# Kernel optimization log

Measured on AMD Instinct MI355X. Metric: run time of the kernel, lower is better.

## Reference

```python
import jax, jax.numpy as jnp
import numpy as np

N_NODES, N_EDGES, NODE_D, EDGE_D, EMB_D, N_GRAPHS = 50000, 800000, 128, 100, 92, 256
N_CONV, FC_D, N_FC, CUTOFF = 3, 128, 2, 6.0


def setup_inputs() -> dict:
    key = jax.random.key(0)
    ks = jax.random.split(key, 24)
    s = 0.05
    inp = {
        "z": jax.random.randint(ks[0], (N_NODES,), 0, 100, dtype=jnp.int32),
        "R": jax.random.normal(ks[1], (N_NODES, 3), dtype=jnp.float32) * 5.0,
        "edge_index": jax.random.randint(ks[2], (2, N_EDGES), 0, N_NODES, dtype=jnp.int32),
        "batch": jnp.sort(jax.random.randint(ks[3], (N_NODES,), 0, N_GRAPHS, dtype=jnp.int32)),
        # learned parameters
        "embedding": jax.random.uniform(ks[4], (100, EMB_D), dtype=jnp.float32),
        "emb_w": jax.random.normal(ks[5], (EMB_D, NODE_D), dtype=jnp.float32) * s,
        "emb_b": jnp.zeros((NODE_D,), jnp.float32),
        "conv_w": jax.random.normal(ks[6], (N_CONV, 2 * NODE_D + EDGE_D, 2 * NODE_D), dtype=jnp.float32) * s,
        "conv_b": jnp.zeros((N_CONV, 2 * NODE_D), jnp.float32),
        "ln_g": jnp.ones((N_CONV, NODE_D), jnp.float32),
        "ln_b": jnp.zeros((N_CONV, NODE_D), jnp.float32),
        "cfc_w": jax.random.normal(ks[7], (NODE_D, FC_D), dtype=jnp.float32) * s,
        "cfc_b": jnp.zeros((FC_D,), jnp.float32),
        "fc_w": jax.random.normal(ks[8], (N_FC, FC_D, FC_D), dtype=jnp.float32) * s,
        "fc_b": jnp.zeros((N_FC, FC_D), jnp.float32),
        "out_w": jax.random.normal(ks[9], (FC_D, 1), dtype=jnp.float32) * s,
        "out_b": jnp.zeros((1,), jnp.float32),
    }
    return inp


def _gaussian_smearing(d):
    offsets = jnp.linspace(0.0, CUTOFF, EDGE_D, dtype=d.dtype)  # [EDGE_D]
    coeff = -0.5 / (offsets[1] - offsets[0]) ** 2
    return jnp.exp(coeff * (d[:, None] - offsets[None, :]) ** 2)  # [E, EDGE_D]


def _layernorm(x, g, b, eps=1e-5):
    mu = x.mean(-1, keepdims=True)
    var = x.var(-1, keepdims=True)
    return (x - mu) / jnp.sqrt(var + eps) * g + b


def reference(z, R, edge_index, batch, embedding, emb_w, emb_b, conv_w, conv_b,
              ln_g, ln_b, cfc_w, cfc_b, fc_w, fc_b, out_w, out_b):
    src, dst = edge_index[0], edge_index[1]  # messages flow src(j) -> dst(i)
    d = jnp.linalg.norm(R[src] - R[dst], axis=-1)  # [E]
    edge_attr = _gaussian_smearing(d)  # [E, EDGE_D]

    x = embedding[z] @ emb_w + emb_b  # [N, NODE_D]
    n = x.shape[0]
    for l in range(conv_w.shape[0]):
        xi, xj = x[dst], x[src]  # gather [E, NODE_D]
        zc = jnp.concatenate([xi, xj, edge_attr], axis=1) @ conv_w[l] + conv_b[l]  # [E, 2*NODE_D]
        z1, z2 = jnp.split(zc, 2, axis=1)
        msg = jax.nn.sigmoid(z1) * jax.nn.softplus(z2)  # [E, NODE_D]
        agg = jax.ops.segment_sum(msg, dst, num_segments=n)  # scatter-add
        x = jax.nn.softplus(_layernorm(agg, ln_g[l], ln_b[l]) + x)

    # global mean pool over graphs
    sums = jax.ops.segment_sum(x, batch, num_segments=N_GRAPHS)
    cnts = jax.ops.segment_sum(jnp.ones((n, 1), x.dtype), batch, num_segments=N_GRAPHS)
    mol = sums / jnp.maximum(cnts, 1.0)  # [N_GRAPHS, NODE_D]

    h = jax.nn.softplus(mol @ cfc_w + cfc_b)
    for l in range(fc_w.shape[0]):
        h = jax.nn.softplus(h @ fc_w[l] + fc_b[l])
    return h @ out_w + out_b  # energy [N_GRAPHS, 1]
```

## Files before the change

kernel.cpp:

```cpp
#include <hip/hip_runtime.h>
#include <hip/hip_bf16.h>
#include <cmath>

#define N_NODES 50000
#define N_EDGES 800000
#define NODE_DIM 128
#define EDGE_DIM 100
#define EMB_DIM 92
#define N_GRAPHS 256

typedef __attribute__((ext_vector_type(8))) short short8_t;
typedef __attribute__((ext_vector_type(4))) float float4_t;

__device__ __forceinline__ float softplus_f(float v) {
    return v > 20.0f ? v : __logf(1.0f + __expf(v));
}
__device__ __forceinline__ float sigmoid_f(float v) {
    return 1.0f / (1.0f + __expf(-v));
}

__global__ void deg_kernel(const int* __restrict__ ei, int* __restrict__ deg) {
    int e = blockIdx.x * blockDim.x + threadIdx.x;
    if (e >= N_EDGES) return;
    atomicAdd(&deg[ei[N_EDGES + e]], 1);
}

#define SB 1024
__global__ void scan1_kernel(const int* __restrict__ deg, int* __restrict__ rp,
                             int* __restrict__ bsum) {
    __shared__ int buf[SB];
    int b = blockIdx.x, t = threadIdx.x, i = b * SB + t;
    int v = (i < N_NODES) ? deg[i] : 0;
    buf[t] = v;
    __syncthreads();
    for (int off = 1; off < SB; off <<= 1) {
        int a = (t >= off) ? buf[t - off] : 0;
        __syncthreads();
        buf[t] += a;
        __syncthreads();
    }
    if (i < N_NODES) rp[i] = buf[t] - v;
    if (t == SB - 1) bsum[b] = buf[t];
}
__global__ void scan2_kernel(int* __restrict__ bsum, int n) {
    if (threadIdx.x == 0) {
        int s = 0;
        for (int i = 0; i < n; i++) { int v = bsum[i]; bsum[i] = s; s += v; }
    }
}
__global__ void scan3_kernel(int* __restrict__ rp, const int* __restrict__ bsum) {
    int i = blockIdx.x * SB + threadIdx.x;
    if (i < N_NODES) rp[i] += bsum[blockIdx.x];
    if (i == 0) rp[N_NODES] = N_EDGES;
}

__global__ void fill_kernel(const int* __restrict__ ei, const float* __restrict__ R,
                            const int* __restrict__ row_ptr, int* __restrict__ cnt2,
                            int* __restrict__ s_src, float* __restrict__ s_d) {
    int e = blockIdx.x * blockDim.x + threadIdx.x;
    if (e >= N_EDGES) return;
    int s = ei[e];
    int dst = ei[N_EDGES + e];
    float dx = R[3 * s + 0] - R[3 * dst + 0];
    float dy = R[3 * s + 1] - R[3 * dst + 1];
    float dz = R[3 * s + 2] - R[3 * dst + 2];
    float d = sqrtf(dx * dx + dy * dy + dz * dz);
    int pos = row_ptr[dst] + atomicAdd(&cnt2[dst], 1);
    s_src[pos] = s;
    s_d[pos] = d;
}

__global__ void gb_kernel(const int* __restrict__ batch, int* __restrict__ gs) {
    int i = blockIdx.x * 256 + threadIdx.x;
    if (i > N_NODES) return;
    int b = (i < N_NODES) ? batch[i] : N_GRAPHS;
    int pb = (i == 0) ? -1 : batch[i - 1];
    for (int g = pb + 1; g <= b; g++) gs[g] = i;
}

__global__ void wcvt_kernel(const float* __restrict__ conv_w, __hip_bfloat16* __restrict__ Webf) {
    int i = blockIdx.x * 256 + threadIdx.x;
    if (i >= 3 * EDGE_DIM * 256) return;
    int l = i / (EDGE_DIM * 256), r = i - l * (EDGE_DIM * 256);
    Webf[i] = (__hip_bfloat16)conv_w[(size_t)l * 356 * 256 + 256 * 256 + r];
}

__global__ void wprep_kernel(const float* __restrict__ conv_w, short* __restrict__ WbB) {
    int idx = blockIdx.x * 256 + threadIdx.x;
    if (idx >= 3 * 4 * 32 * 64 * 8) return;
    int j = idx & 7;
    int lane = (idx >> 3) & 63;
    int nt = (idx >> 9) & 31;
    int kc = (idx >> 14) & 3;
    int l = idx >> 16;
    int k = kc * 32 + (lane >> 4) * 8 + j;
    int nl = lane & 15;
    int row, col;
    if (nt < 16) { row = k; col = nt * 16 + nl; }
    else { row = 128 + k; col = (nt - 16) * 16 + nl; }
    __hip_bfloat16 bv = (__hip_bfloat16)conv_w[(size_t)l * 356 * 256 + (size_t)row * 256 + col];
    WbB[idx] = *(short*)&bv;
}

__global__ void embed_kernel(const int* __restrict__ z, const float* __restrict__ emb,
                             const float* __restrict__ emb_w, const float* __restrict__ emb_b,
                             float* __restrict__ x, __hip_bfloat16* __restrict__ xb) {
    __shared__ float er[EMB_DIM * 8];
    __shared__ int zi[8];
    int base = blockIdx.x * 8;
    int t = threadIdx.x;
    if (t < 8) zi[t] = z[base + t];
    __syncthreads();
    for (int idx = t; idx < EMB_DIM * 8; idx += 128) {
        int k = idx >> 3, j = idx & 7;
        er[idx] = emb[zi[j] * EMB_DIM + k];
    }
    __syncthreads();
    float acc[8];
    float bb = emb_b[t];
#pragma unroll
    for (int j = 0; j < 8; j++) acc[j] = bb;
    for (int k = 0; k < EMB_DIM; k++) {
        float w = emb_w[k * NODE_DIM + t];
        float4 ja = *(const float4*)&er[k * 8];
        float4 jb = *(const float4*)&er[k * 8 + 4];
        acc[0] = fmaf(w, ja.x, acc[0]); acc[1] = fmaf(w, ja.y, acc[1]);
        acc[2] = fmaf(w, ja.z, acc[2]); acc[3] = fmaf(w, ja.w, acc[3]);
        acc[4] = fmaf(w, jb.x, acc[4]); acc[5] = fmaf(w, jb.y, acc[5]);
        acc[6] = fmaf(w, jb.z, acc[6]); acc[7] = fmaf(w, jb.w, acc[7]);
    }
#pragma unroll
    for (int j = 0; j < 8; j++) {
        x[(base + j) * NODE_DIM + t] = acc[j];
        xb[(base + j) * NODE_DIM + t] = (__hip_bfloat16)acc[j];
    }
}

__global__ __launch_bounds__(256) void node_mfma_kernel(
    const __hip_bfloat16* __restrict__ xb, const short* __restrict__ WbB,
    const float* __restrict__ bl, float* __restrict__ P1, float* __restrict__ P2) {
    int t = threadIdx.x;
    int wv = t >> 6, lane = t & 63;
    int mrow = lane & 15, q = lane >> 4;
    int base = blockIdx.x * 16;
    const short* xr = (const short*)xb + (size_t)(base + mrow) * 128 + q * 8;
    float4_t acc[8];
#pragma unroll
    for (int i = 0; i < 8; i++) acc[i] = (float4_t){0.f, 0.f, 0.f, 0.f};
#pragma unroll
    for (int kc = 0; kc < 4; kc++) {
        short8_t a = *(const short8_t*)(xr + kc * 32);
#pragma unroll
        for (int i = 0; i < 8; i++) {
            int nt = wv * 8 + i;
            short8_t b = *(const short8_t*)&WbB[((size_t)(kc * 32 + nt) * 64 + lane) * 8];
            acc[i] = __builtin_amdgcn_mfma_f32_16x16x32_bf16(a, b, acc[i], 0, 0, 0);
        }
    }
#pragma unroll
    for (int i = 0; i < 8; i++) {
        int nt = wv * 8 + i;
        int np = nt * 16 + mrow;
        if (np < 256) {
            float bb = bl[np];
#pragma unroll
            for (int r = 0; r < 4; r++)
                P1[(size_t)(base + q * 4 + r) * 256 + np] = acc[i][r] + bb;
        } else {
#pragma unroll
            for (int r = 0; r < 4; r++)
                P2[(size_t)(base + q * 4 + r) * 256 + (np - 256)] = acc[i][r];
        }
    }
}

#define NTAP 10
__device__ __forceinline__ float edge_msg(float b1, float b2, float dv,
                                          float a1, float a2,
                                          const __hip_bfloat16* __restrict__ Wc) {
    const float sp_ = 6.0f / 99.0f;
    const float inv_s = 99.0f / 6.0f;
    const float coeff = -0.5f * inv_s * inv_s;
    float z1 = a1 + b1, z2 = a2 + b2;
    if (dv <= 6.34f) {
        int k0 = max(0, min(EDGE_DIM - NTAP, (int)ceilf(dv * inv_s - 4.5f)));
        const __hip_bfloat16* wr = Wc + k0 * 256;
#pragma unroll
        for (int i = 0; i < NTAP; i++) {
            float df = dv - (float)(k0 + i) * sp_;
            float ee = __expf(coeff * df * df);
            z1 = fmaf((float)wr[i * 256], ee, z1);
            z2 = fmaf((float)wr[i * 256 + 128], ee, z2);
        }
    }
    return sigmoid_f(z1) * softplus_f(z2);
}

__global__ __launch_bounds__(256) void node_edge_ln_kernel(
    const int* __restrict__ row_ptr, const int* __restrict__ s_src,
    const float* __restrict__ s_d, const float* __restrict__ P1,
    const float* __restrict__ P2, const __hip_bfloat16* __restrict__ We,
    const float* __restrict__ lg, const float* __restrict__ lb,
    float* __restrict__ x, __hip_bfloat16* __restrict__ xb) {
    int node = blockIdx.x * 2 + (threadIdx.x >> 7);
    int c = threadIdx.x & 127;
    int e0 = row_ptr[node], e1 = row_ptr[node + 1];
    float a1 = P1[(size_t)node * 256 + c];
    float a2 = P1[(size_t)node * 256 + 128 + c];
    const __hip_bfloat16* Wc = We + c;
    float acc = 0.f;
    float b1A = 0.f, b2A = 0.f, dvA = 0.f;
    float b1B = 0.f, b2B = 0.f, dvB = 0.f;
    int srcC = 0, srcD = 0;
    float dC = 0.f, dD = 0.f;
    if (e0 < e1) {
        int s = s_src[e0]; dvA = s_d[e0];
        b1A = P2[(size_t)s * 256 + c]; b2A = P2[(size_t)s * 256 + 128 + c];
    }
    if (e0 + 1 < e1) {
        int s = s_src[e0 + 1]; dvB = s_d[e0 + 1];
        b1B = P2[(size_t)s * 256 + c]; b2B = P2[(size_t)s * 256 + 128 + c];
    }
    if (e0 + 2 < e1) { srcC = s_src[e0 + 2]; dC = s_d[e0 + 2]; }
    if (e0 + 3 < e1) { srcD = s_src[e0 + 3]; dD = s_d[e0 + 3]; }
    int e = e0;
    while (e < e1) {
        {
            float b1 = b1A, b2 = b2A, dv = dvA;
            if (e + 2 < e1) {
                b1A = P2[(size_t)srcC * 256 + c];
                b2A = P2[(size_t)srcC * 256 + 128 + c];
                dvA = dC;
            }
            if (e + 4 < e1) { srcC = s_src[e + 4]; dC = s_d[e + 4]; }
            acc += edge_msg(b1, b2, dv, a1, a2, Wc);
        }
        e++;
        if (e >= e1) break;
        {
            float b1 = b1B, b2 = b2B, dv = dvB;
            if (e + 2 < e1) {
                b1B = P2[(size_t)srcD * 256 + c];
                b2B = P2[(size_t)srcD * 256 + 128 + c];
                dvB = dD;
            }
            if (e + 4 < e1) { srcD = s_src[e + 4]; dD = s_d[e + 4]; }
            acc += edge_msg(b1, b2, dv, a1, a2, Wc);
        }
        e++;
    }
    __shared__ float sm[4][2];
    float s1 = acc, s2 = acc * acc;
#pragma unroll
    for (int off = 32; off > 0; off >>= 1) {
        s1 += __shfl_xor(s1, off);
        s2 += __shfl_xor(s2, off);
    }
    int wv = threadIdx.x >> 6;
    if ((threadIdx.x & 63) == 0) { sm[wv][0] = s1; sm[wv][1] = s2; }
    __syncthreads();
    int w0 = (threadIdx.x >> 7) * 2;
    float S1 = sm[w0][0] + sm[w0 + 1][0];
    float S2 = sm[w0][1] + sm[w0 + 1][1];
    float mu = S1 * (1.0f / 128.0f);
    float var = S2 * (1.0f / 128.0f) - mu * mu;
    float rstd = rsqrtf(fmaxf(var, 0.f) + 1e-5f);
    float xv = x[(size_t)node * 128 + c];
    float res = softplus_f((acc - mu) * rstd * lg[c] + lb[c] + xv);
    x[(size_t)node * 128 + c] = res;
    xb[(size_t)node * 128 + c] = (__hip_bfloat16)res;
}

__global__ void pool_head_kernel(const float* __restrict__ x, const int* __restrict__ gs,
                                 const float* __restrict__ cfc_w, const float* __restrict__ cfc_b,
                                 const float* __restrict__ fc_w, const float* __restrict__ fc_b,
                                 const float* __restrict__ out_w, const float* __restrict__ out_b,
                                 float* __restrict__ out) {
    int g = blockIdx.x, c = threadIdx.x;
    int n0 = gs[g], n1 = gs[g + 1];
    float s = 0.f;
    for (int n = n0; n < n1; n++) s += x[(size_t)n * 128 + c];
    __shared__ float h[128], h2[128];
    h[c] = s / fmaxf((float)(n1 - n0), 1.0f);
    __syncthreads();
    float acc = cfc_b[c];
    for (int k = 0; k < 128; k++) acc = fmaf(h[k], cfc_w[k * 128 + c], acc);
    h2[c] = softplus_f(acc);
    __syncthreads();
    for (int l = 0; l < 2; l++) {
        const float* W = fc_w + l * 128 * 128;
        acc = fc_b[l * 128 + c];
        for (int k = 0; k < 128; k++) acc = fmaf(h2[k], W[k * 128 + c], acc);
        __syncthreads();
        h2[c] = softplus_f(acc);
        __syncthreads();
    }
    h[c] = h2[c] * out_w[c];
    __syncthreads();
    for (int off = 64; off > 0; off >>= 1) {
        if (c < off) h[c] += h[c + off];
        __syncthreads();
    }
    if (c == 0) out[g] = h[0] + out_b[0];
}

extern "C" void kernel_launch(void* const* d_in, const int* in_sizes, int n_in,
                              void* d_out, int out_size, void* d_ws, size_t ws_size,
                              hipStream_t stream) {
    const int*   z      = (const int*)d_in[0];
    const float* R      = (const float*)d_in[1];
    const int*   ei     = (const int*)d_in[2];
    const int*   batch  = (const int*)d_in[3];
    const float* emb    = (const float*)d_in[4];
    const float* emb_w  = (const float*)d_in[5];
    const float* emb_b  = (const float*)d_in[6];
    const float* conv_w = (const float*)d_in[7];
    const float* conv_b = (const float*)d_in[8];
    const float* ln_g   = (const float*)d_in[9];
    const float* ln_b   = (const float*)d_in[10];
    const float* cfc_w  = (const float*)d_in[11];
    const float* cfc_b  = (const float*)d_in[12];
    const float* fc_w   = (const float*)d_in[13];
    const float* fc_b   = (const float*)d_in[14];
    const float* out_w  = (const float*)d_in[15];
    const float* out_b  = (const float*)d_in[16];
    float* out = (float*)d_out;

    float* ws    = (float*)d_ws;
    float* x     = ws;
    float* agg   = x + 6400000;
    float* P1    = agg + 6400000;
    float* P2    = P1 + 12800000;
    float* s_d   = P2 + 12800000;
    int* s_src   = (int*)(s_d + 800000);
    int* s_dst   = s_src + 800000;
    int* row_ptr = s_dst + 800000;
    int* deg     = row_ptr + 50004;
    int* cnt2    = deg + 50000;
    int* bsum    = cnt2 + 50000;
    int* gs      = bsum + 64;
    __hip_bfloat16* Webf = (__hip_bfloat16*)(gs + 260);
    short* WbB           = (short*)(Webf + 76800);
    __hip_bfloat16* xb   = (__hip_bfloat16*)(WbB + 196608);

    hipMemsetAsync(deg, 0, (size_t)100000 * 4, stream);
    deg_kernel<<<(N_EDGES + 255) / 256, 256, 0, stream>>>(ei, deg);
    int nsb = (N_NODES + SB - 1) / SB;
    scan1_kernel<<<nsb, SB, 0, stream>>>(deg, row_ptr, bsum);
    scan2_kernel<<<1, 64, 0, stream>>>(bsum, nsb);
    scan3_kernel<<<nsb, SB, 0, stream>>>(row_ptr, bsum);
    fill_kernel<<<(N_EDGES + 255) / 256, 256, 0, stream>>>(ei, R, row_ptr, cnt2,
                                                           s_src, s_d);
    gb_kernel<<<(N_NODES + 256) / 256 + 1, 256, 0, stream>>>(batch, gs);
    wcvt_kernel<<<(3 * EDGE_DIM * 256 + 255) / 256, 256, 0, stream>>>(conv_w, Webf);
    wprep_kernel<<<(3 * 4 * 32 * 64 * 8 + 255) / 256, 256, 0, stream>>>(conv_w, WbB);

    embed_kernel<<<N_NODES / 8, 128, 0, stream>>>(z, emb, emb_w, emb_b, x, xb);
    for (int l = 0; l < 3; l++) {
        node_mfma_kernel<<<N_NODES / 16, 256, 0, stream>>>(xb, WbB + (size_t)l * 65536,
                                                           conv_b + l * 256, P1, P2);
        node_edge_ln_kernel<<<N_NODES / 2, 256, 0, stream>>>(
            row_ptr, s_src, s_d, P1, P2, Webf + (size_t)l * EDGE_DIM * 256,
            ln_g + l * 128, ln_b + l * 128, x, xb);
    }
    pool_head_kernel<<<N_GRAPHS, 128, 0, stream>>>(x, gs, cfc_w, cfc_b, fc_w, fc_b,
                                                   out_w, out_b, out);
}
```

Baseline: 914.0 us.

## Interleave gate/filter projections, pack edge metadata and paired bf16 weights

The node projection outputs P1/P2 are now stored with the z1 and z2 halves interleaved per channel, so the edge kernel fetches both with one float2 gather instead of two scalar gathers per source node. Edge source index and distance are packed into a single float2 array, and the edge-attribute weights for both halves are packed into one 32-bit word of two bf16 values. The aim is fewer memory transactions in the latency-bound gather loop. In exchange the writes from the MFMA kernel are strided more irregularly, and the weight and metadata preparation kernels change accordingly.

```diff
diff --git a/kernel.cpp b/kernel.cpp
--- a/kernel.cpp
+++ b/kernel.cpp
@@ -18,6 +18,8 @@
 __device__ __forceinline__ float sigmoid_f(float v) {
     return 1.0f / (1.0f + __expf(-v));
 }
+__device__ __forceinline__ float bflo(unsigned u) { return __uint_as_float(u << 16); }
+__device__ __forceinline__ float bfhi(unsigned u) { return __uint_as_float(u & 0xffff0000u); }
 
 __global__ void deg_kernel(const int* __restrict__ ei, int* __restrict__ deg) {
     int e = blockIdx.x * blockDim.x + threadIdx.x;
@@ -56,7 +58,7 @@
 
 __global__ void fill_kernel(const int* __restrict__ ei, const float* __restrict__ R,
                             const int* __restrict__ row_ptr, int* __restrict__ cnt2,
-                            int* __restrict__ s_src, float* __restrict__ s_d) {
+                            float2* __restrict__ em) {
     int e = blockIdx.x * blockDim.x + threadIdx.x;
     if (e >= N_EDGES) return;
     int s = ei[e];
@@ -66,8 +68,7 @@
     float dz = R[3 * s + 2] - R[3 * dst + 2];
     float d = sqrtf(dx * dx + dy * dy + dz * dz);
     int pos = row_ptr[dst] + atomicAdd(&cnt2[dst], 1);
-    s_src[pos] = s;
-    s_d[pos] = d;
+    em[pos] = make_float2(__int_as_float(s), d);
 }
 
 __global__ void gb_kernel(const int* __restrict__ batch, int* __restrict__ gs) {
@@ -78,11 +79,15 @@
     for (int g = pb + 1; g <= b; g++) gs[g] = i;
 }
 
-__global__ void wcvt_kernel(const float* __restrict__ conv_w, __hip_bfloat16* __restrict__ Webf) {
+__global__ void wcvt_kernel(const float* __restrict__ conv_w, unsigned* __restrict__ Wep) {
     int i = blockIdx.x * 256 + threadIdx.x;
-    if (i >= 3 * EDGE_DIM * 256) return;
-    int l = i / (EDGE_DIM * 256), r = i - l * (EDGE_DIM * 256);
-    Webf[i] = (__hip_bfloat16)conv_w[(size_t)l * 356 * 256 + 256 * 256 + r];
+    if (i >= 3 * EDGE_DIM * 128) return;
+    int l = i / (EDGE_DIM * 128), r = i - l * (EDGE_DIM * 128);
+    int k = r >> 7, c = r & 127;
+    const float* row = conv_w + (size_t)l * 356 * 256 + (size_t)(256 + k) * 256;
+    __hip_bfloat16 lo = (__hip_bfloat16)row[c];
+    __hip_bfloat16 hi = (__hip_bfloat16)row[128 + c];
+    Wep[i] = ((unsigned)*(unsigned short*)&hi << 16) | (unsigned)*(unsigned short*)&lo;
 }
 
 __global__ void wprep_kernel(const float* __restrict__ conv_w, short* __restrict__ WbB) {
@@ -138,7 +143,7 @@
 
 __global__ __launch_bounds__(256) void node_mfma_kernel(
     const __hip_bfloat16* __restrict__ xb, const short* __restrict__ WbB,
-    const float* __restrict__ bl, float* __restrict__ P1, float* __restrict__ P2) {
+    const float* __restrict__ bl, float* __restrict__ P1f, float* __restrict__ P2f) {
     int t = threadIdx.x;
     int wv = t >> 6, lane = t & 63;
     int mrow = lane & 15, q = lane >> 4;
@@ -163,101 +168,98 @@
         int np = nt * 16 + mrow;
         if (np < 256) {
             float bb = bl[np];
+            int off = 2 * (np & 127) + (np >> 7);
 #pragma unroll
             for (int r = 0; r < 4; r++)
-                P1[(size_t)(base + q * 4 + r) * 256 + np] = acc[i][r] + bb;
+                P1f[(size_t)(base + q * 4 + r) * 256 + off] = acc[i][r] + bb;
         } else {
+            int np2 = np - 256;
+            int off = 2 * (np2 & 127) + (np2 >> 7);
 #pragma unroll
             for (int r = 0; r < 4; r++)
-                P2[(size_t)(base + q * 4 + r) * 256 + (np - 256)] = acc[i][r];
+                P2f[(size_t)(base + q * 4 + r) * 256 + off] = acc[i][r];
         }
     }
 }
 
 #define NTAP 10
-__device__ __forceinline__ float edge_msg(float b1, float b2, float dv,
-                                          float a1, float a2,
-                                          const __hip_bfloat16* __restrict__ Wc) {
+__device__ __forceinline__ float edge_msg(float2 b, float dv, float a1, float a2,
+                                          const unsigned* __restrict__ Wc) {
     const float sp_ = 6.0f / 99.0f;
     const float inv_s = 99.0f / 6.0f;
     const float coeff = -0.5f * inv_s * inv_s;
-    float z1 = a1 + b1, z2 = a2 + b2;
+    float z1 = a1 + b.x, z2 = a2 + b.y;
     if (dv <= 6.34f) {
         int k0 = max(0, min(EDGE_DIM - NTAP, (int)ceilf(dv * inv_s - 4.5f)));
-        const __hip_bfloat16* wr = Wc + k0 * 256;
+        const unsigned* wr = Wc + k0 * 128;
 #pragma unroll
         for (int i = 0; i < NTAP; i++) {
             float df = dv - (float)(k0 + i) * sp_;
             float ee = __expf(coeff * df * df);
-            z1 = fmaf((float)wr[i * 256], ee, z1);
-            z2 = fmaf((float)wr[i * 256 + 128], ee, z2);
+            unsigned u = wr[i * 128];
+            z1 = fmaf(bflo(u), ee, z1);
+            z2 = fmaf(bfhi(u), ee, z2);
         }
     }
     return sigmoid_f(z1) * softplus_f(z2);
 }
 
 __global__ __launch_bounds__(256) void node_edge_ln_kernel(
-    const int* __restrict__ row_ptr, const int* __restrict__ s_src,
-    const float* __restrict__ s_d, const float* __restrict__ P1,
-    const float* __restrict__ P2, const __hip_bfloat16* __restrict__ We,
+    const int* __restrict__ row_ptr, const float2* __restrict__ em,
+    const float2* __restrict__ P1p, const float2* __restrict__ P2p,
+    const unsigned* __restrict__ Wep,
     const float* __restrict__ lg, const float* __restrict__ lb,
     float* __restrict__ x, __hip_bfloat16* __restrict__ xb) {
     int node = blockIdx.x * 2 + (threadIdx.x >> 7);
     int c = threadIdx.x & 127;
     int e0 = row_ptr[node], e1 = row_ptr[node + 1];
-    float a1 = P1[(size_t)node * 256 + c];
-    float a2 = P1[(size_t)node * 256 + 128 + c];
-    const __hip_bfloat16* Wc = We + c;
+    float2 av = P1p[(size_t)node * 128 + c];
+    float a1 = av.x, a2 = av.y;
+    const unsigned* Wc = Wep + c;
     float acc = 0.f;
-    float b1A = 0.f, b2A = 0.f, dvA = 0.f;
-    float b1B = 0.f, b2B = 0.f, dvB = 0.f;
+    float2 bA = make_float2(0.f, 0.f), bB = make_float2(0.f, 0.f);
+    float dvA = 0.f, dvB = 0.f;
     int srcC = 0, srcD = 0;
     float dC = 0.f, dD = 0.f;
     if (e0 < e1) {
-        int s = s_src[e0]; dvA = s_d[e0];
-        b1A = P2[(size_t)s * 256 + c]; b2A = P2[(size_t)s * 256 + 128 + c];
+        float2 m = em[e0];
+        int s = __float_as_int(m.x); dvA = m.y;
+        bA = P2p[(size_t)s * 128 + c];
     }
     if (e0 + 1 < e1) {
-        int s = s_src[e0 + 1]; dvB = s_d[e0 + 1];
-        b1B = P2[(size_t)s * 256 + c]; b2B = P2[(size_t)s * 256 + 128 + c];
-    }
-    if (e0 + 2 < e1) { srcC = s_src[e0 + 2]; dC = s_d[e0 + 2]; }
-    if (e0 + 3 < e1) { srcD = s_src[e0 + 3]; dD = s_d[e0 + 3]; }
+        float2 m = em[e0 + 1];
+        int s = __float_as_int(m.x); dvB = m.y;
+        bB = P2p[(size_t)s * 128 + c];
+    }
+    if (e0 + 2 < e1) { float2 m = em[e0 + 2]; srcC = __float_as_int(m.x); dC = m.y; }
+    if (e0 + 3 < e1) { float2 m = em[e0 + 3]; srcD = __float_as_int(m.x); dD = m.y; }
     int e = e0;
     while (e < e1) {
         {
-            float b1 = b1A, b2 = b2A, dv = dvA;
-            if (e + 2 < e1) {
-                b1A = P2[(size_t)srcC * 256 + c];
-                b2A = P2[(size_t)srcC * 256 + 128 + c];
-                dvA = dC;
-            }
-            if (e + 4 < e1) { srcC = s_src[e + 4]; dC = s_d[e + 4]; }
-            acc += edge_msg(b1, b2, dv, a1, a2, Wc);
+            float2 b = bA; float dv = dvA;
+            if (e + 2 < e1) { bA = P2p[(size_t)srcC * 128 + c]; dvA = dC; }
+            if (e + 4 < e1) { float2 m = em[e + 4]; srcC = __float_as_int(m.x); dC = m.y; }
+            acc += edge_msg(b, dv, a1, a2, Wc);
         }
         e++;
         if (e >= e1) break;
         {
-            float b1 = b1B, b2 = b2B, dv = dvB;
-            if (e + 2 < e1) {
-                b1B = P2[(size_t)srcD * 256 + c];
-                b2B = P2[(size_t)srcD * 256 + 128 + c];
-                dvB = dD;
-            }
-            if (e + 4 < e1) { srcD = s_src[e + 4]; dD = s_d[e + 4]; }
-            acc += edge_msg(b1, b2, dv, a1, a2, Wc);
+            float2 b = bB; float dv = dvB;
+            if (e + 2 < e1) { bB = P2p[(size_t)srcD * 128 + c]; dvB = dD; }
+            if (e + 4 < e1) { float2 m = em[e + 4]; srcD = __float_as_int(m.x); dD = m.y; }
+            acc += edge_msg(b, dv, a1, a2, Wc);
         }
         e++;
     }
     __shared__ float sm[4][2];
-    float s1 = acc, s2 = acc * acc;
+    float s1r = acc, s2r = acc * acc;
 #pragma unroll
     for (int off = 32; off > 0; off >>= 1) {
-        s1 += __shfl_xor(s1, off);
-        s2 += __shfl_xor(s2, off);
+        s1r += __shfl_xor(s1r, off);
+        s2r += __shfl_xor(s2r, off);
     }
     int wv = threadIdx.x >> 6;
-    if ((threadIdx.x & 63) == 0) { sm[wv][0] = s1; sm[wv][1] = s2; }
+    if ((threadIdx.x & 63) == 0) { sm[wv][0] = s1r; sm[wv][1] = s2r; }
     __syncthreads();
     int w0 = (threadIdx.x >> 7) * 2;
     float S1 = sm[w0][0] + sm[w0 + 1][0];
@@ -329,19 +331,19 @@
     float* ws    = (float*)d_ws;
     float* x     = ws;
     float* agg   = x + 6400000;
-    float* P1    = agg + 6400000;
-    float* P2    = P1 + 12800000;
-    float* s_d   = P2 + 12800000;
-    int* s_src   = (int*)(s_d + 800000);
-    int* s_dst   = s_src + 800000;
+    float* P1f   = agg + 6400000;
+    float* P2f   = P1f + 12800000;
+    float* emf   = P2f + 12800000;
+    int* s_dst   = (int*)(emf + 1600000);
     int* row_ptr = s_dst + 800000;
     int* deg     = row_ptr + 50004;
     int* cnt2    = deg + 50000;
     int* bsum    = cnt2 + 50000;
     int* gs      = bsum + 64;
-    __hip_bfloat16* Webf = (__hip_bfloat16*)(gs + 260);
-    short* WbB           = (short*)(Webf + 76800);
+    unsigned* Wep        = (unsigned*)(gs + 260);
+    short* WbB           = (short*)(Wep + 38400);
     __hip_bfloat16* xb   = (__hip_bfloat16*)(WbB + 196608);
+    float2* em = (float2*)emf;
 
     hipMemsetAsync(deg, 0, (size_t)100000 * 4, stream);
     deg_kernel<<<(N_EDGES + 255) / 256, 256, 0, stream>>>(ei, deg);
@@ -349,18 +351,18 @@
     scan1_kernel<<<nsb, SB, 0, stream>>>(deg, row_ptr, bsum);
     scan2_kernel<<<1, 64, 0, stream>>>(bsum, nsb);
     scan3_kernel<<<nsb, SB, 0, stream>>>(row_ptr, bsum);
-    fill_kernel<<<(N_EDGES + 255) / 256, 256, 0, stream>>>(ei, R, row_ptr, cnt2,
-                                                           s_src, s_d);
+    fill_kernel<<<(N_EDGES + 255) / 256, 256, 0, stream>>>(ei, R, row_ptr, cnt2, em);
     gb_kernel<<<(N_NODES + 256) / 256 + 1, 256, 0, stream>>>(batch, gs);
-    wcvt_kernel<<<(3 * EDGE_DIM * 256 + 255) / 256, 256, 0, stream>>>(conv_w, Webf);
+    wcvt_kernel<<<(3 * EDGE_DIM * 128 + 255) / 256, 256, 0, stream>>>(conv_w, Wep);
     wprep_kernel<<<(3 * 4 * 32 * 64 * 8 + 255) / 256, 256, 0, stream>>>(conv_w, WbB);
 
     embed_kernel<<<N_NODES / 8, 128, 0, stream>>>(z, emb, emb_w, emb_b, x, xb);
     for (int l = 0; l < 3; l++) {
         node_mfma_kernel<<<N_NODES / 16, 256, 0, stream>>>(xb, WbB + (size_t)l * 65536,
-                                                           conv_b + l * 256, P1, P2);
+                                                           conv_b + l * 256, P1f, P2f);
         node_edge_ln_kernel<<<N_NODES / 2, 256, 0, stream>>>(
-            row_ptr, s_src, s_d, P1, P2, Webf + (size_t)l * EDGE_DIM * 256,
+            row_ptr, em, (const float2*)P1f, (const float2*)P2f,
+            Wep + (size_t)l * EDGE_DIM * 128,
             ln_g + l * 128, ln_b + l * 128, x, xb);
     }
     pool_head_kernel<<<N_GRAPHS, 128, 0, stream>>>(x, gs, cfc_w, cfc_b, fc_w, fc_b,
```

Result: slower. 1.009 ms (+10.4%).
